# Optimization experiments

Hardware: AMD Instinct MI355X
Metric: run time of the kernel (lower is better)

The kernel has to match this reference:

```python
import jax, jax.numpy as jnp
import numpy as np

N_NODES = 100_000
N_EDGES = 1_600_000
N_FEAT = 64
E_FEAT = 32
OUT_FEAT = 64


def _xavier_normal(key, shape, gain):
    fan_out, fan_in = shape
    std = gain * np.sqrt(2.0 / (fan_in + fan_out))
    return jax.random.normal(key, shape, dtype=jnp.float32) * std


def setup_inputs() -> dict:
    key = jax.random.key(0)
    ks = jax.random.split(key, 9)
    d_cat = 2 * N_FEAT + E_FEAT  # 160
    n_feat = jax.random.normal(ks[0], (N_NODES, N_FEAT), dtype=jnp.float32)
    e_feat = jax.random.normal(ks[1], (N_EDGES, E_FEAT), dtype=jnp.float32)
    src = jax.random.randint(ks[2], (N_EDGES,), 0, N_NODES, dtype=jnp.int32)
    dst = jax.random.randint(ks[3], (N_EDGES,), 0, N_NODES, dtype=jnp.int32)
    gain = np.sqrt(2.0)
    bound_msg = 1.0 / np.sqrt(d_cat)
    return {
        "n_feat": n_feat,
        "e_feat": e_feat,
        "src": src,
        "dst": dst,
        # W_msg uses default torch Linear init (kaiming-uniform-ish); exact init irrelevant for correctness
        "W_msg_w": jax.random.uniform(ks[4], (OUT_FEAT, d_cat), jnp.float32, -bound_msg, bound_msg),
        "W_msg_b": jax.random.uniform(ks[5], (OUT_FEAT,), jnp.float32, -bound_msg, bound_msg),
        # W uses xavier_normal with gain sqrt(2)
        "W_w": _xavier_normal(ks[6], (2 * OUT_FEAT, d_cat), gain),
        "W_b": jax.random.uniform(ks[7], (2 * OUT_FEAT,), jnp.float32, -bound_msg, bound_msg),
        "a": _xavier_normal(ks[8], (2 * OUT_FEAT, 1), gain),
    }


def reference(n_feat, e_feat, src, dst, W_msg_w, W_msg_b, W_w, W_b, a):
    # gather: per-edge concat [E, 2*n_feat + e_feat]
    feat_cat = jnp.concatenate([n_feat[src], n_feat[dst], e_feat], axis=1)
    # edge attention logits: leaky_relu((feat_cat @ W^T + b) @ a)  -> [E]
    w_feat = feat_cat @ W_w.T + W_b                      # [E, 2*out_feat]
    logits = jax.nn.leaky_relu(w_feat @ a[:, 0])         # [E]
    # edge softmax grouped by destination node
    seg_max = jax.ops.segment_max(logits, dst, num_segments=N_NODES)  # [N]
    ex = jnp.exp(logits - seg_max[dst])                  # [E]
    seg_sum = jax.ops.segment_sum(ex, dst, num_segments=N_NODES)     # [N]
    att = ex / seg_sum[dst]                              # [E]
    # messages and weighted scatter-sum aggregation
    msg = feat_cat @ W_msg_w.T + W_msg_b                 # [E, out_feat]
    agg = jax.ops.segment_sum(att[:, None] * msg, dst, num_segments=N_NODES)  # [N, out_feat]
    return jax.nn.relu(agg)
```

## Files before the change

### kernel.cpp

```cpp
#include <hip/hip_runtime.h>
#include <hip/hip_bf16.h>

#define N_NODES 100000
#define N_EDGES 1600000
#define NF 64
#define EF 32

#define SCAN_B 512
#define SCAN_NB ((N_NODES + SCAN_B - 1) / SCAN_B)


__global__ __launch_bounds__(256) void k0_prep(
    const float* __restrict__ Ww, const float* __restrict__ Wb,
    const float* __restrict__ a, const float* __restrict__ Wmsg,
    float* __restrict__ v, float* __restrict__ W1T, float* __restrict__ W2T,
    float* __restrict__ WmeT) {
  int t = threadIdx.x;
  for (int j = t; j < 160; j += 256) {
    float s = 0.f;
    for (int k = 0; k < 128; ++k) s = fmaf(a[k], Ww[k * 160 + j], s);
    v[j] = s;
  }
  if (t == 0) {
    float s = 0.f;
    for (int k = 0; k < 128; ++k) s = fmaf(a[k], Wb[k], s);
    v[160] = s;
  }
  for (int idx = t; idx < 64 * 64; idx += 256) {
    int j = idx >> 6, i = idx & 63;
    W1T[idx] = Wmsg[i * 160 + j];
    W2T[idx] = Wmsg[i * 160 + 64 + j];
  }
  for (int idx = t; idx < 32 * 64; idx += 256) {
    int j = idx >> 6, i = idx & 63;
    WmeT[idx] = Wmsg[i * 160 + 128 + j];
  }
}

__global__ __launch_bounds__(256) void k1_node(
    const float* __restrict__ nf_g, const float* __restrict__ v,
    const float* __restrict__ W1T, const float* __restrict__ W2T,
    float* __restrict__ s1, float* __restrict__ s2,
    float* __restrict__ m_src, float* __restrict__ m_dst) {
  int n = blockIdx.x * 256 + threadIdx.x;
  if (n >= N_NODES) return;
  const float4* nf4 = (const float4*)(nf_g + (size_t)n * NF);
  float acc[64];
#pragma unroll
  for (int i = 0; i < 64; ++i) acc[i] = 0.f;
  float s1a = 0.f, s2a = 0.f;
  for (int j4 = 0; j4 < 16; ++j4) {
    float4 q = nf4[j4];
    float xs[4] = {q.x, q.y, q.z, q.w};
#pragma unroll
    for (int u = 0; u < 4; ++u) {
      int j = j4 * 4 + u;
      float x = xs[u];
      s1a = fmaf(v[j], x, s1a);
      s2a = fmaf(v[64 + j], x, s2a);
      const float* w = W1T + j * 64;
#pragma unroll
      for (int i = 0; i < 64; ++i) acc[i] = fmaf(w[i], x, acc[i]);
    }
  }
  s1[n] = s1a;
  s2[n] = s2a;
  float* ms = m_src + (size_t)n * NF;
#pragma unroll
  for (int i = 0; i < 64; ++i) ms[i] = acc[i];
#pragma unroll
  for (int i = 0; i < 64; ++i) acc[i] = 0.f;
  for (int j4 = 0; j4 < 16; ++j4) {
    float4 q = nf4[j4];
    float xs[4] = {q.x, q.y, q.z, q.w};
#pragma unroll
    for (int u = 0; u < 4; ++u) {
      int j = j4 * 4 + u;
      float x = xs[u];
      const float* w = W2T + j * 64;
#pragma unroll
      for (int i = 0; i < 64; ++i) acc[i] = fmaf(w[i], x, acc[i]);
    }
  }
  float* md = m_dst + (size_t)n * NF;
#pragma unroll
  for (int i = 0; i < 64; ++i) md[i] = acc[i];
}

__global__ __launch_bounds__(256) void k_count(const int* __restrict__ dst,
                                               int* __restrict__ cnt) {
  int e = blockIdx.x * 256 + threadIdx.x;
  if (e < N_EDGES) atomicAdd(&cnt[dst[e]], 1);
}

__global__ __launch_bounds__(SCAN_B) void kS1(const int* __restrict__ cnt,
                                              int* __restrict__ bsum) {
  __shared__ int sh[SCAN_B];
  int t = threadIdx.x;
  int i = blockIdx.x * SCAN_B + t;
  sh[t] = (i < N_NODES) ? cnt[i] : 0;
  __syncthreads();
  for (int d = SCAN_B / 2; d > 0; d >>= 1) {
    if (t < d) sh[t] += sh[t + d];
    __syncthreads();
  }
  if (t == 0) bsum[blockIdx.x] = sh[0];
}

__global__ __launch_bounds__(256) void kS2(const int* __restrict__ bsum,
                                           int* __restrict__ boff,
                                           int* __restrict__ row_ptr) {
  __shared__ int sh[256];
  int t = threadIdx.x;
  sh[t] = (t < SCAN_NB) ? bsum[t] : 0;
  __syncthreads();
  for (int d = 1; d < 256; d <<= 1) {
    int val = (t >= d) ? sh[t - d] : 0;
    __syncthreads();
    sh[t] += val;
    __syncthreads();
  }
  if (t < SCAN_NB) boff[t] = (t == 0) ? 0 : sh[t - 1];
  if (t == 255) row_ptr[N_NODES] = sh[255];
}

__global__ __launch_bounds__(SCAN_B) void kS3(const int* __restrict__ cnt,
                                              const int* __restrict__ boff,
                                              int* __restrict__ row_ptr,
                                              int* __restrict__ cursor) {
  __shared__ int sh[SCAN_B];
  int t = threadIdx.x;
  int i = blockIdx.x * SCAN_B + t;
  int val = (i < N_NODES) ? cnt[i] : 0;
  sh[t] = val;
  __syncthreads();
  for (int d = 1; d < SCAN_B; d <<= 1) {
    int u = (t >= d) ? sh[t - d] : 0;
    __syncthreads();
    sh[t] += u;
    __syncthreads();
  }
  if (i < N_NODES) {
    int excl = boff[blockIdx.x] + sh[t] - val;
    row_ptr[i] = excl;
    cursor[i] = excl;
  }
}

__global__ __launch_bounds__(256) void kE_scatter(
    const int* __restrict__ src, const int* __restrict__ dst,
    const float* __restrict__ e_feat, const float* __restrict__ s1,
    const float* __restrict__ s2, const float* __restrict__ v,
    int* __restrict__ cursor, unsigned long long* __restrict__ edata) {
  int e = blockIdx.x * 256 + threadIdx.x;
  if (e >= N_EDGES) return;
  int sn = src[e], dn = dst[e];
  const float4* efr = (const float4*)(e_feat + (size_t)e * EF);
  float t = 0.f;
#pragma unroll
  for (int i = 0; i < 8; ++i) {
    float4 q = efr[i];
    t = fmaf(q.x, v[128 + i * 4 + 0], t);
    t = fmaf(q.y, v[128 + i * 4 + 1], t);
    t = fmaf(q.z, v[128 + i * 4 + 2], t);
    t = fmaf(q.w, v[128 + i * 4 + 3], t);
  }
  float lg = s1[sn] + s2[dn] + t + v[160];
  float l = lg > 0.f ? lg : 0.01f * lg;
  float ex = __expf(l);
  int p = atomicAdd(&cursor[dn], 1);
  unsigned long long pk = ((unsigned long long)(unsigned)e << 43) |
                          ((unsigned long long)(unsigned)sn << 26) |
                          (unsigned long long)(__float_as_uint(ex) >> 6);
  edata[p] = pk;
}

__global__ __launch_bounds__(256) void k3_agg(
    const int* __restrict__ row_ptr, const int2* __restrict__ edata,
    const float* __restrict__ e_feat, const float* __restrict__ m_src,
    const float* __restrict__ m_dst, const float* __restrict__ WmeT,
    const float* __restrict__ Wmsg_b, float* __restrict__ out) {
  int lane = threadIdx.x & 63;
  int wid = threadIdx.x >> 6;
  int n = blockIdx.x * 4 + wid;
  if (n >= N_NODES) return;
  int start = row_ptr[n];
  int end = row_ptr[n + 1];
  int half = lane >> 5;
  int col = lane & 31;
  float sum_ex = 0.f, acc_ms = 0.f, acc_ef = 0.f;
  for (int base = start; base < end; base += 64) {
    int2 md = make_int2(0, 0);
    if (base + lane < end) md = edata[base + lane];
    int m = end - base;
    if (m > 64) m = 64;
    int mm4 = (m + 3) & ~3;
    for (int k = 0; k < mm4; k += 4) {
      int ek[4], sk[4];
      float exk[4], msk[4], efh[2], exh[2];
#pragma unroll
      for (int u = 0; u < 4; ++u) {
        unsigned lo = (unsigned)__shfl(md.x, k + u);
        unsigned hi = (unsigned)__shfl(md.y, k + u);
        ek[u] = (int)(hi >> 11);
        sk[u] = (int)(((hi & 0x7FFu) << 6) | (lo >> 26));
        exk[u] = __uint_as_float((lo & 0x3FFFFFFu) << 6);
      }
      int eh0 = half ? ek[1] : ek[0];
      int eh1 = half ? ek[3] : ek[2];
      exh[0] = half ? exk[1] : exk[0];
      exh[1] = half ? exk[3] : exk[2];
#pragma unroll
      for (int u = 0; u < 4; ++u)
        msk[u] = m_src[(size_t)sk[u] * NF + lane];
      efh[0] = e_feat[(size_t)eh0 * EF + col];
      efh[1] = e_feat[(size_t)eh1 * EF + col];
#pragma unroll
      for (int u = 0; u < 4; ++u) {
        sum_ex += exk[u];
        acc_ms = fmaf(exk[u], msk[u], acc_ms);
      }
      acc_ef = fmaf(exh[0], efh[0], acc_ef);
      acc_ef = fmaf(exh[1], efh[1], acc_ef);
    }
  }
  float mm = 0.f;
#pragma unroll
  for (int j = 0; j < 32; ++j) {
    float efj = __shfl(acc_ef, j) + __shfl(acc_ef, j + 32);
    mm = fmaf(WmeT[j * 64 + lane], efj, mm);
  }
  float o = 0.f;
  if (sum_ex > 0.f) {
    o = (acc_ms + mm) / sum_ex + m_dst[(size_t)n * NF + lane] + Wmsg_b[lane];
    o = fmaxf(o, 0.f);
  }
  out[(size_t)n * NF + lane] = o;
}

extern "C" void kernel_launch(void* const* d_in, const int* in_sizes, int n_in,
                              void* d_out, int out_size, void* d_ws,
                              size_t ws_size, hipStream_t stream) {
  const float* n_feat = (const float*)d_in[0];
  const float* e_feat = (const float*)d_in[1];
  const int* src = (const int*)d_in[2];
  const int* dst = (const int*)d_in[3];
  const float* Wmsg_w = (const float*)d_in[4];
  const float* Wmsg_b = (const float*)d_in[5];
  const float* W_w = (const float*)d_in[6];
  const float* W_b = (const float*)d_in[7];
  const float* a = (const float*)d_in[8];
  float* out = (float*)d_out;

  char* ws = (char*)d_ws;
  size_t off = 0;
  auto alloc = [&](size_t bytes) -> char* {
    char* p = ws + off;
    off = (off + bytes + 255) & ~(size_t)255;
    return p;
  };
  float* v = (float*)alloc(161 * 4);
  float* W1T = (float*)alloc(64 * 64 * 4);
  float* W2T = (float*)alloc(64 * 64 * 4);
  float* WmeT = (float*)alloc(32 * 64 * 4);
  float* s1 = (float*)alloc(N_NODES * 4);
  float* s2 = (float*)alloc(N_NODES * 4);
  float* m_src = (float*)alloc((size_t)N_NODES * NF * 4);
  float* m_dst = (float*)alloc((size_t)N_NODES * NF * 4);
  int* cnt = (int*)alloc(N_NODES * 4);
  int* row_ptr = (int*)alloc((N_NODES + 1) * 4);
  int* cursor = (int*)alloc(N_NODES * 4);
  int* bsum = (int*)alloc(SCAN_NB * 4);
  int* boff = (int*)alloc(SCAN_NB * 4);
  unsigned long long* edata = (unsigned long long*)alloc((size_t)N_EDGES * 8);
  if (off > ws_size) return;

  k0_prep<<<1, 256, 0, stream>>>(W_w, W_b, a, Wmsg_w, v, W1T, W2T, WmeT);
  k1_node<<<(N_NODES + 255) / 256, 256, 0, stream>>>(n_feat, v, W1T, W2T, s1,
                                                     s2, m_src, m_dst);
  hipMemsetAsync(cnt, 0, N_NODES * 4, stream);
  k_count<<<(N_EDGES + 255) / 256, 256, 0, stream>>>(dst, cnt);
  kS1<<<SCAN_NB, SCAN_B, 0, stream>>>(cnt, bsum);
  kS2<<<1, 256, 0, stream>>>(bsum, boff, row_ptr);
  kS3<<<SCAN_NB, SCAN_B, 0, stream>>>(cnt, boff, row_ptr, cursor);
  kE_scatter<<<(N_EDGES + 255) / 256, 256, 0, stream>>>(src, dst, e_feat, s1,
                                                        s2, v, cursor, edata);
  k3_agg<<<(N_NODES + 3) / 4, 256, 0, stream>>>(row_ptr, (const int2*)edata,
                                                e_feat, m_src, m_dst, WmeT,
                                                Wmsg_b, out);
}
```

Before: 627.9 us.

## Store m_src and CSR-sorted edge features in fp16 for the aggregation gather

Stores the per-node source message projection as fp16 instead of fp32. The scatter kernel now also writes each edge's features as fp16 into CSR order, so the aggregation kernel reads them contiguously instead of gathering e_feat by edge id. The packed edge record drops the edge id and keeps the full fp32 exp value. This cuts random-gather bytes in the aggregation kernel at the cost of an extra 100MB write in scatter and fp16 rounding error.

```diff
diff --git a/kernel.cpp b/kernel.cpp
--- a/kernel.cpp
+++ b/kernel.cpp
@@ -1,5 +1,6 @@
 #include <hip/hip_runtime.h>
 #include <hip/hip_bf16.h>
+#include <hip/hip_fp16.h>
 
 #define N_NODES 100000
 #define N_EDGES 1600000
@@ -9,6 +10,11 @@
 #define SCAN_B 512
 #define SCAN_NB ((N_NODES + SCAN_B - 1) / SCAN_B)
 
+
+__device__ __forceinline__ unsigned pkh2(float a, float b) {
+  __half2 h = __floats2half2_rn(a, b);
+  return *reinterpret_cast<unsigned*>(&h);
+}
 
 __global__ __launch_bounds__(256) void k0_prep(
     const float* __restrict__ Ww, const float* __restrict__ Wb,
@@ -41,7 +47,7 @@
     const float* __restrict__ nf_g, const float* __restrict__ v,
     const float* __restrict__ W1T, const float* __restrict__ W2T,
     float* __restrict__ s1, float* __restrict__ s2,
-    float* __restrict__ m_src, float* __restrict__ m_dst) {
+    __half* __restrict__ m_src_h, float* __restrict__ m_dst) {
   int n = blockIdx.x * 256 + threadIdx.x;
   if (n >= N_NODES) return;
   const float4* nf4 = (const float4*)(nf_g + (size_t)n * NF);
@@ -65,9 +71,13 @@
   }
   s1[n] = s1a;
   s2[n] = s2a;
-  float* ms = m_src + (size_t)n * NF;
-#pragma unroll
-  for (int i = 0; i < 64; ++i) ms[i] = acc[i];
+  uint4* ms4 = (uint4*)(m_src_h + (size_t)n * NF);
+#pragma unroll
+  for (int b = 0; b < 8; ++b)
+    ms4[b] = make_uint4(pkh2(acc[b * 8 + 0], acc[b * 8 + 1]),
+                        pkh2(acc[b * 8 + 2], acc[b * 8 + 3]),
+                        pkh2(acc[b * 8 + 4], acc[b * 8 + 5]),
+                        pkh2(acc[b * 8 + 6], acc[b * 8 + 7]));
 #pragma unroll
   for (int i = 0; i < 64; ++i) acc[i] = 0.f;
   for (int j4 = 0; j4 < 16; ++j4) {
@@ -151,33 +161,41 @@
     const int* __restrict__ src, const int* __restrict__ dst,
     const float* __restrict__ e_feat, const float* __restrict__ s1,
     const float* __restrict__ s2, const float* __restrict__ v,
-    int* __restrict__ cursor, unsigned long long* __restrict__ edata) {
+    int* __restrict__ cursor, unsigned long long* __restrict__ edata,
+    __half* __restrict__ ef_s) {
   int e = blockIdx.x * 256 + threadIdx.x;
   if (e >= N_EDGES) return;
   int sn = src[e], dn = dst[e];
   const float4* efr = (const float4*)(e_feat + (size_t)e * EF);
+  float4 q[8];
+#pragma unroll
+  for (int i = 0; i < 8; ++i) q[i] = efr[i];
   float t = 0.f;
 #pragma unroll
   for (int i = 0; i < 8; ++i) {
-    float4 q = efr[i];
-    t = fmaf(q.x, v[128 + i * 4 + 0], t);
-    t = fmaf(q.y, v[128 + i * 4 + 1], t);
-    t = fmaf(q.z, v[128 + i * 4 + 2], t);
-    t = fmaf(q.w, v[128 + i * 4 + 3], t);
+    t = fmaf(q[i].x, v[128 + i * 4 + 0], t);
+    t = fmaf(q[i].y, v[128 + i * 4 + 1], t);
+    t = fmaf(q[i].z, v[128 + i * 4 + 2], t);
+    t = fmaf(q[i].w, v[128 + i * 4 + 3], t);
   }
   float lg = s1[sn] + s2[dn] + t + v[160];
   float l = lg > 0.f ? lg : 0.01f * lg;
   float ex = __expf(l);
   int p = atomicAdd(&cursor[dn], 1);
-  unsigned long long pk = ((unsigned long long)(unsigned)e << 43) |
-                          ((unsigned long long)(unsigned)sn << 26) |
-                          (unsigned long long)(__float_as_uint(ex) >> 6);
-  edata[p] = pk;
+  edata[p] = ((unsigned long long)(unsigned)sn << 32) |
+             (unsigned long long)__float_as_uint(ex);
+  uint4* o4 = (uint4*)(ef_s + (size_t)p * EF);
+#pragma unroll
+  for (int i = 0; i < 4; ++i)
+    o4[i] = make_uint4(pkh2(q[2 * i].x, q[2 * i].y),
+                       pkh2(q[2 * i].z, q[2 * i].w),
+                       pkh2(q[2 * i + 1].x, q[2 * i + 1].y),
+                       pkh2(q[2 * i + 1].z, q[2 * i + 1].w));
 }
 
 __global__ __launch_bounds__(256) void k3_agg(
     const int* __restrict__ row_ptr, const int2* __restrict__ edata,
-    const float* __restrict__ e_feat, const float* __restrict__ m_src,
+    const __half* __restrict__ ef_s, const __half* __restrict__ m_src_h,
     const float* __restrict__ m_dst, const float* __restrict__ WmeT,
     const float* __restrict__ Wmsg_b, float* __restrict__ out) {
   int lane = threadIdx.x & 63;
@@ -186,9 +204,10 @@
   if (n >= N_NODES) return;
   int start = row_ptr[n];
   int end = row_ptr[n + 1];
-  int half = lane >> 5;
-  int col = lane & 31;
-  float sum_ex = 0.f, acc_ms = 0.f, acc_ef = 0.f;
+  int g = lane >> 4;
+  int c2 = lane & 15;
+  float sum_ex = 0.f, acc_ms = 0.f;
+  float aefx = 0.f, aefy = 0.f;
   for (int base = start; base < end; base += 64) {
     int2 md = make_int2(0, 0);
     if (base + lane < end) md = edata[base + lane];
@@ -196,39 +215,42 @@
     if (m > 64) m = 64;
     int mm4 = (m + 3) & ~3;
     for (int k = 0; k < mm4; k += 4) {
-      int ek[4], sk[4];
-      float exk[4], msk[4], efh[2], exh[2];
-#pragma unroll
-      for (int u = 0; u < 4; ++u) {
-        unsigned lo = (unsigned)__shfl(md.x, k + u);
-        unsigned hi = (unsigned)__shfl(md.y, k + u);
-        ek[u] = (int)(hi >> 11);
-        sk[u] = (int)(((hi & 0x7FFu) << 6) | (lo >> 26));
-        exk[u] = __uint_as_float((lo & 0x3FFFFFFu) << 6);
-      }
-      int eh0 = half ? ek[1] : ek[0];
-      int eh1 = half ? ek[3] : ek[2];
-      exh[0] = half ? exk[1] : exk[0];
-      exh[1] = half ? exk[3] : exk[2];
-#pragma unroll
-      for (int u = 0; u < 4; ++u)
-        msk[u] = m_src[(size_t)sk[u] * NF + lane];
-      efh[0] = e_feat[(size_t)eh0 * EF + col];
-      efh[1] = e_feat[(size_t)eh1 * EF + col];
-#pragma unroll
-      for (int u = 0; u < 4; ++u) {
-        sum_ex += exk[u];
-        acc_ms = fmaf(exk[u], msk[u], acc_ms);
-      }
-      acc_ef = fmaf(exh[0], efh[0], acc_ef);
-      acc_ef = fmaf(exh[1], efh[1], acc_ef);
+      float ex0 = __uint_as_float((unsigned)__shfl(md.x, k + 0));
+      float ex1 = __uint_as_float((unsigned)__shfl(md.x, k + 1));
+      float ex2 = __uint_as_float((unsigned)__shfl(md.x, k + 2));
+      float ex3 = __uint_as_float((unsigned)__shfl(md.x, k + 3));
+      int s0 = __shfl(md.y, k + 0);
+      int s1i = __shfl(md.y, k + 1);
+      int s2i = __shfl(md.y, k + 2);
+      int s3 = __shfl(md.y, k + 3);
+      float exg = (g == 0) ? ex0 : (g == 1) ? ex1 : (g == 2) ? ex2 : ex3;
+      const __half2* ep =
+          (const __half2*)(ef_s + ((size_t)(base + k + g)) * EF + c2 * 2);
+      float2 ef2 = __half22float2(*ep);
+      aefx = fmaf(exg, ef2.x, aefx);
+      aefy = fmaf(exg, ef2.y, aefy);
+      float ms0 = __half2float(m_src_h[(size_t)s0 * NF + lane]);
+      float ms1 = __half2float(m_src_h[(size_t)s1i * NF + lane]);
+      float ms2 = __half2float(m_src_h[(size_t)s2i * NF + lane]);
+      float ms3 = __half2float(m_src_h[(size_t)s3 * NF + lane]);
+      sum_ex += (ex0 + ex1) + (ex2 + ex3);
+      acc_ms = fmaf(ex0, ms0, acc_ms);
+      acc_ms = fmaf(ex1, ms1, acc_ms);
+      acc_ms = fmaf(ex2, ms2, acc_ms);
+      acc_ms = fmaf(ex3, ms3, acc_ms);
     }
   }
+  aefx += __shfl_xor(aefx, 16);
+  aefx += __shfl_xor(aefx, 32);
+  aefy += __shfl_xor(aefy, 16);
+  aefy += __shfl_xor(aefy, 32);
   float mm = 0.f;
 #pragma unroll
-  for (int j = 0; j < 32; ++j) {
-    float efj = __shfl(acc_ef, j) + __shfl(acc_ef, j + 32);
-    mm = fmaf(WmeT[j * 64 + lane], efj, mm);
+  for (int jp = 0; jp < 16; ++jp) {
+    float ea = __shfl(aefx, jp);
+    float eb = __shfl(aefy, jp);
+    mm = fmaf(WmeT[(2 * jp) * 64 + lane], ea, mm);
+    mm = fmaf(WmeT[(2 * jp + 1) * 64 + lane], eb, mm);
   }
   float o = 0.f;
   if (sum_ex > 0.f) {
@@ -265,7 +287,7 @@
   float* WmeT = (float*)alloc(32 * 64 * 4);
   float* s1 = (float*)alloc(N_NODES * 4);
   float* s2 = (float*)alloc(N_NODES * 4);
-  float* m_src = (float*)alloc((size_t)N_NODES * NF * 4);
+  __half* m_src_h = (__half*)alloc((size_t)N_NODES * NF * 2);
   float* m_dst = (float*)alloc((size_t)N_NODES * NF * 4);
   int* cnt = (int*)alloc(N_NODES * 4);
   int* row_ptr = (int*)alloc((N_NODES + 1) * 4);
@@ -273,19 +295,21 @@
   int* bsum = (int*)alloc(SCAN_NB * 4);
   int* boff = (int*)alloc(SCAN_NB * 4);
   unsigned long long* edata = (unsigned long long*)alloc((size_t)N_EDGES * 8);
+  __half* ef_s = (__half*)alloc(((size_t)N_EDGES + 8) * EF * 2);
   if (off > ws_size) return;
 
   k0_prep<<<1, 256, 0, stream>>>(W_w, W_b, a, Wmsg_w, v, W1T, W2T, WmeT);
   k1_node<<<(N_NODES + 255) / 256, 256, 0, stream>>>(n_feat, v, W1T, W2T, s1,
-                                                     s2, m_src, m_dst);
+                                                     s2, m_src_h, m_dst);
   hipMemsetAsync(cnt, 0, N_NODES * 4, stream);
   k_count<<<(N_EDGES + 255) / 256, 256, 0, stream>>>(dst, cnt);
   kS1<<<SCAN_NB, SCAN_B, 0, stream>>>(cnt, bsum);
   kS2<<<1, 256, 0, stream>>>(bsum, boff, row_ptr);
   kS3<<<SCAN_NB, SCAN_B, 0, stream>>>(cnt, boff, row_ptr, cursor);
   kE_scatter<<<(N_EDGES + 255) / 256, 256, 0, stream>>>(src, dst, e_feat, s1,
-                                                        s2, v, cursor, edata);
+                                                        s2, v, cursor, edata,
+                                                        ef_s);
   k3_agg<<<(N_NODES + 3) / 4, 256, 0, stream>>>(row_ptr, (const int2*)edata,
-                                                e_feat, m_src, m_dst, WmeT,
+                                                ef_s, m_src_h, m_dst, WmeT,
                                                 Wmsg_b, out);
 }
```

Result: no change. 627.5 us (-0.1%).

## Replace CSR sort-and-gather aggregation with fused per-edge atomic scatter

Applied to the files above, without the earlier changes.

Drops the count/scan/scatter CSR build and the per-node gather kernel. Each wavefront now handles two edges at a time: it computes the logit and exp, then atomically adds ex-weighted source messages, edge features and the exp sum into per-node fp32 accumulators, and a final kernel normalises and applies the edge-feature projection. The source-node message table is stored in fp16 to halve gather traffic. The cost is about 100 float atomics per edge (64 message columns, 32 edge-feature columns and the sum), fp16 rounding of the messages, and the max-free exp is kept as before.

```diff
diff --git a/kernel.cpp b/kernel.cpp
--- a/kernel.cpp
+++ b/kernel.cpp
@@ -1,14 +1,17 @@
 #include <hip/hip_runtime.h>
 #include <hip/hip_bf16.h>
+#include <hip/hip_fp16.h>
 
 #define N_NODES 100000
 #define N_EDGES 1600000
 #define NF 64
 #define EF 32
 
-#define SCAN_B 512
-#define SCAN_NB ((N_NODES + SCAN_B - 1) / SCAN_B)
-
+
+__device__ __forceinline__ unsigned pkh2(float a, float b) {
+  __half2 h = __floats2half2_rn(a, b);
+  return *reinterpret_cast<unsigned*>(&h);
+}
 
 __global__ __launch_bounds__(256) void k0_prep(
     const float* __restrict__ Ww, const float* __restrict__ Wb,
@@ -41,7 +44,7 @@
     const float* __restrict__ nf_g, const float* __restrict__ v,
     const float* __restrict__ W1T, const float* __restrict__ W2T,
     float* __restrict__ s1, float* __restrict__ s2,
-    float* __restrict__ m_src, float* __restrict__ m_dst) {
+    __half* __restrict__ m_src_h, float* __restrict__ m_dst) {
   int n = blockIdx.x * 256 + threadIdx.x;
   if (n >= N_NODES) return;
   const float4* nf4 = (const float4*)(nf_g + (size_t)n * NF);
@@ -65,9 +68,13 @@
   }
   s1[n] = s1a;
   s2[n] = s2a;
-  float* ms = m_src + (size_t)n * NF;
-#pragma unroll
-  for (int i = 0; i < 64; ++i) ms[i] = acc[i];
+  uint4* ms4 = (uint4*)(m_src_h + (size_t)n * NF);
+#pragma unroll
+  for (int b = 0; b < 8; ++b)
+    ms4[b] = make_uint4(pkh2(acc[b * 8 + 0], acc[b * 8 + 1]),
+                        pkh2(acc[b * 8 + 2], acc[b * 8 + 3]),
+                        pkh2(acc[b * 8 + 4], acc[b * 8 + 5]),
+                        pkh2(acc[b * 8 + 6], acc[b * 8 + 7]));
 #pragma unroll
   for (int i = 0; i < 64; ++i) acc[i] = 0.f;
   for (int j4 = 0; j4 < 16; ++j4) {
@@ -87,152 +94,66 @@
   for (int i = 0; i < 64; ++i) md[i] = acc[i];
 }
 
-__global__ __launch_bounds__(256) void k_count(const int* __restrict__ dst,
-                                               int* __restrict__ cnt) {
-  int e = blockIdx.x * 256 + threadIdx.x;
-  if (e < N_EDGES) atomicAdd(&cnt[dst[e]], 1);
-}
-
-__global__ __launch_bounds__(SCAN_B) void kS1(const int* __restrict__ cnt,
-                                              int* __restrict__ bsum) {
-  __shared__ int sh[SCAN_B];
-  int t = threadIdx.x;
-  int i = blockIdx.x * SCAN_B + t;
-  sh[t] = (i < N_NODES) ? cnt[i] : 0;
-  __syncthreads();
-  for (int d = SCAN_B / 2; d > 0; d >>= 1) {
-    if (t < d) sh[t] += sh[t + d];
-    __syncthreads();
-  }
-  if (t == 0) bsum[blockIdx.x] = sh[0];
-}
-
-__global__ __launch_bounds__(256) void kS2(const int* __restrict__ bsum,
-                                           int* __restrict__ boff,
-                                           int* __restrict__ row_ptr) {
-  __shared__ int sh[256];
-  int t = threadIdx.x;
-  sh[t] = (t < SCAN_NB) ? bsum[t] : 0;
-  __syncthreads();
-  for (int d = 1; d < 256; d <<= 1) {
-    int val = (t >= d) ? sh[t - d] : 0;
-    __syncthreads();
-    sh[t] += val;
-    __syncthreads();
-  }
-  if (t < SCAN_NB) boff[t] = (t == 0) ? 0 : sh[t - 1];
-  if (t == 255) row_ptr[N_NODES] = sh[255];
-}
-
-__global__ __launch_bounds__(SCAN_B) void kS3(const int* __restrict__ cnt,
-                                              const int* __restrict__ boff,
-                                              int* __restrict__ row_ptr,
-                                              int* __restrict__ cursor) {
-  __shared__ int sh[SCAN_B];
-  int t = threadIdx.x;
-  int i = blockIdx.x * SCAN_B + t;
-  int val = (i < N_NODES) ? cnt[i] : 0;
-  sh[t] = val;
-  __syncthreads();
-  for (int d = 1; d < SCAN_B; d <<= 1) {
-    int u = (t >= d) ? sh[t - d] : 0;
-    __syncthreads();
-    sh[t] += u;
-    __syncthreads();
-  }
-  if (i < N_NODES) {
-    int excl = boff[blockIdx.x] + sh[t] - val;
-    row_ptr[i] = excl;
-    cursor[i] = excl;
-  }
-}
-
-__global__ __launch_bounds__(256) void kE_scatter(
-    const int* __restrict__ src, const int* __restrict__ dst,
+__global__ __launch_bounds__(256) void kE_fused(
+    const int2* __restrict__ src2, const int2* __restrict__ dst2,
     const float* __restrict__ e_feat, const float* __restrict__ s1,
     const float* __restrict__ s2, const float* __restrict__ v,
-    int* __restrict__ cursor, unsigned long long* __restrict__ edata) {
-  int e = blockIdx.x * 256 + threadIdx.x;
-  if (e >= N_EDGES) return;
-  int sn = src[e], dn = dst[e];
-  const float4* efr = (const float4*)(e_feat + (size_t)e * EF);
-  float t = 0.f;
-#pragma unroll
-  for (int i = 0; i < 8; ++i) {
-    float4 q = efr[i];
-    t = fmaf(q.x, v[128 + i * 4 + 0], t);
-    t = fmaf(q.y, v[128 + i * 4 + 1], t);
-    t = fmaf(q.z, v[128 + i * 4 + 2], t);
-    t = fmaf(q.w, v[128 + i * 4 + 3], t);
-  }
-  float lg = s1[sn] + s2[dn] + t + v[160];
-  float l = lg > 0.f ? lg : 0.01f * lg;
-  float ex = __expf(l);
-  int p = atomicAdd(&cursor[dn], 1);
-  unsigned long long pk = ((unsigned long long)(unsigned)e << 43) |
-                          ((unsigned long long)(unsigned)sn << 26) |
-                          (unsigned long long)(__float_as_uint(ex) >> 6);
-  edata[p] = pk;
-}
-
-__global__ __launch_bounds__(256) void k3_agg(
-    const int* __restrict__ row_ptr, const int2* __restrict__ edata,
-    const float* __restrict__ e_feat, const float* __restrict__ m_src,
-    const float* __restrict__ m_dst, const float* __restrict__ WmeT,
-    const float* __restrict__ Wmsg_b, float* __restrict__ out) {
+    const __half* __restrict__ m_src_h, float* __restrict__ sum_ex,
+    float* __restrict__ acc_ef, float* __restrict__ acc_ms) {
+  int lane = threadIdx.x & 63;
+  int wv = (blockIdx.x * 256 + threadIdx.x) >> 6;
+  int nw = (gridDim.x * 256) >> 6;
+  int half = lane >> 5;
+  int hl = lane & 31;
+  float vv = v[128 + hl];
+  float cb = v[160];
+  for (int p = wv; p < N_EDGES / 2; p += nw) {
+    int2 sp = src2[p];
+    int2 dp = dst2[p];
+    int sn = half ? sp.y : sp.x;
+    int dn = half ? dp.y : dp.x;
+    float ef = e_feat[(size_t)p * 64 + lane];
+    float t = ef * vv;
+    t += __shfl_xor(t, 1);
+    t += __shfl_xor(t, 2);
+    t += __shfl_xor(t, 4);
+    t += __shfl_xor(t, 8);
+    t += __shfl_xor(t, 16);
+    float lg = s1[sn] + s2[dn] + t + cb;
+    float l = lg > 0.f ? lg : 0.01f * lg;
+    float ex = __expf(l);
+    float ms0 = __half2float(m_src_h[(size_t)sp.x * NF + lane]);
+    float ms1 = __half2float(m_src_h[(size_t)sp.y * NF + lane]);
+    atomicAdd(&acc_ef[(size_t)dn * EF + hl], ex * ef);
+    if (hl == 0) atomicAdd(&sum_ex[dn], ex);
+    float ex0 = __shfl(ex, 0);
+    float ex1 = __shfl(ex, 32);
+    atomicAdd(&acc_ms[(size_t)dp.x * NF + lane], ex0 * ms0);
+    atomicAdd(&acc_ms[(size_t)dp.y * NF + lane], ex1 * ms1);
+  }
+}
+
+__global__ __launch_bounds__(256) void k4_final(
+    const float* __restrict__ sum_ex, const float* __restrict__ acc_ef,
+    const float* __restrict__ acc_ms, const float* __restrict__ m_dst,
+    const float* __restrict__ WmeT, const float* __restrict__ Wmsg_b,
+    float* __restrict__ out) {
   int lane = threadIdx.x & 63;
   int wid = threadIdx.x >> 6;
   int n = blockIdx.x * 4 + wid;
   if (n >= N_NODES) return;
-  int start = row_ptr[n];
-  int end = row_ptr[n + 1];
-  int half = lane >> 5;
-  int col = lane & 31;
-  float sum_ex = 0.f, acc_ms = 0.f, acc_ef = 0.f;
-  for (int base = start; base < end; base += 64) {
-    int2 md = make_int2(0, 0);
-    if (base + lane < end) md = edata[base + lane];
-    int m = end - base;
-    if (m > 64) m = 64;
-    int mm4 = (m + 3) & ~3;
-    for (int k = 0; k < mm4; k += 4) {
-      int ek[4], sk[4];
-      float exk[4], msk[4], efh[2], exh[2];
-#pragma unroll
-      for (int u = 0; u < 4; ++u) {
-        unsigned lo = (unsigned)__shfl(md.x, k + u);
-        unsigned hi = (unsigned)__shfl(md.y, k + u);
-        ek[u] = (int)(hi >> 11);
-        sk[u] = (int)(((hi & 0x7FFu) << 6) | (lo >> 26));
-        exk[u] = __uint_as_float((lo & 0x3FFFFFFu) << 6);
-      }
-      int eh0 = half ? ek[1] : ek[0];
-      int eh1 = half ? ek[3] : ek[2];
-      exh[0] = half ? exk[1] : exk[0];
-      exh[1] = half ? exk[3] : exk[2];
-#pragma unroll
-      for (int u = 0; u < 4; ++u)
-        msk[u] = m_src[(size_t)sk[u] * NF + lane];
-      efh[0] = e_feat[(size_t)eh0 * EF + col];
-      efh[1] = e_feat[(size_t)eh1 * EF + col];
-#pragma unroll
-      for (int u = 0; u < 4; ++u) {
-        sum_ex += exk[u];
-        acc_ms = fmaf(exk[u], msk[u], acc_ms);
-      }
-      acc_ef = fmaf(exh[0], efh[0], acc_ef);
-      acc_ef = fmaf(exh[1], efh[1], acc_ef);
-    }
-  }
+  float se = sum_ex[n];
+  float af = acc_ef[(size_t)n * EF + (lane & 31)];
+  float am = acc_ms[(size_t)n * NF + lane];
   float mm = 0.f;
 #pragma unroll
   for (int j = 0; j < 32; ++j) {
-    float efj = __shfl(acc_ef, j) + __shfl(acc_ef, j + 32);
-    mm = fmaf(WmeT[j * 64 + lane], efj, mm);
+    float aj = __shfl(af, j);
+    mm = fmaf(WmeT[j * 64 + lane], aj, mm);
   }
   float o = 0.f;
-  if (sum_ex > 0.f) {
-    o = (acc_ms + mm) / sum_ex + m_dst[(size_t)n * NF + lane] + Wmsg_b[lane];
+  if (se > 0.f) {
+    o = (am + mm) / se + m_dst[(size_t)n * NF + lane] + Wmsg_b[lane];
     o = fmaxf(o, 0.f);
   }
   out[(size_t)n * NF + lane] = o;
@@ -265,27 +186,22 @@
   float* WmeT = (float*)alloc(32 * 64 * 4);
   float* s1 = (float*)alloc(N_NODES * 4);
   float* s2 = (float*)alloc(N_NODES * 4);
-  float* m_src = (float*)alloc((size_t)N_NODES * NF * 4);
+  __half* m_src_h = (__half*)alloc((size_t)N_NODES * NF * 2);
   float* m_dst = (float*)alloc((size_t)N_NODES * NF * 4);
-  int* cnt = (int*)alloc(N_NODES * 4);
-  int* row_ptr = (int*)alloc((N_NODES + 1) * 4);
-  int* cursor = (int*)alloc(N_NODES * 4);
-  int* bsum = (int*)alloc(SCAN_NB * 4);
-  int* boff = (int*)alloc(SCAN_NB * 4);
-  unsigned long long* edata = (unsigned long long*)alloc((size_t)N_EDGES * 8);
+  char* zstart = ws + off;
+  float* sum_ex = (float*)alloc(N_NODES * 4);
+  float* acc_ef = (float*)alloc((size_t)N_NODES * EF * 4);
+  float* acc_ms = (float*)alloc((size_t)N_NODES * NF * 4);
+  size_t zbytes = (size_t)((ws + off) - zstart);
   if (off > ws_size) return;
 
+  hipMemsetAsync(zstart, 0, zbytes, stream);
   k0_prep<<<1, 256, 0, stream>>>(W_w, W_b, a, Wmsg_w, v, W1T, W2T, WmeT);
   k1_node<<<(N_NODES + 255) / 256, 256, 0, stream>>>(n_feat, v, W1T, W2T, s1,
-                                                     s2, m_src, m_dst);
-  hipMemsetAsync(cnt, 0, N_NODES * 4, stream);
-  k_count<<<(N_EDGES + 255) / 256, 256, 0, stream>>>(dst, cnt);
-  kS1<<<SCAN_NB, SCAN_B, 0, stream>>>(cnt, bsum);
-  kS2<<<1, 256, 0, stream>>>(bsum, boff, row_ptr);
-  kS3<<<SCAN_NB, SCAN_B, 0, stream>>>(cnt, boff, row_ptr, cursor);
-  kE_scatter<<<(N_EDGES + 255) / 256, 256, 0, stream>>>(src, dst, e_feat, s1,
-                                                        s2, v, cursor, edata);
-  k3_agg<<<(N_NODES + 3) / 4, 256, 0, stream>>>(row_ptr, (const int2*)edata,
-                                                e_feat, m_src, m_dst, WmeT,
-                                                Wmsg_b, out);
-}
+                                                     s2, m_src_h, m_dst);
+  kE_fused<<<1024, 256, 0, stream>>>((const int2*)src, (const int2*)dst,
+                                     e_feat, s1, s2, v, m_src_h, sum_ex,
+                                     acc_ef, acc_ms);
+  k4_final<<<(N_NODES + 3) / 4, 256, 0, stream>>>(sum_ex, acc_ef, acc_ms,
+                                                  m_dst, WmeT, Wmsg_b, out);
+}
```

Result: slower. 921.9 us (+46.8%).
